# Kernel optimization log

Measured on AMD Instinct MI355X. Metric: run time of the kernel, lower is better.

## Reference

```python
import jax, jax.numpy as jnp
import numpy as np

DIM = 512
D_STATE = 16
D_CONV = 4
EXPAND = 2
D_INNER = EXPAND * DIM
DT_RANK = (DIM + 15) // 16  # ceil(dim/16) = 32
B_SZ, SEQ = 2, 2048


def _silu(v):
    return v * jax.nn.sigmoid(v)


def _mamba(x, in_w, conv_w, conv_b, xproj_w, dt_w, dt_b, A_log, D, out_w):
    """Single Mamba block forward (mamba_ssm reference math).
    x: [B, L, d_model]
    """
    Bb, L, _ = x.shape
    d_inner = conv_w.shape[0]
    d_state = A_log.shape[1]
    dt_rank = dt_w.shape[1]

    xz = x @ in_w.T                          # [B, L, 2*d_inner]
    xi, z = jnp.split(xz, 2, axis=-1)

    # causal depthwise conv1d (kernel D_CONV) + SiLU
    K = conv_w.shape[-1]
    xp = jnp.pad(xi, ((0, 0), (K - 1, 0), (0, 0)))
    xc = conv_b + sum(xp[:, k:k + L, :] * conv_w[:, 0, k] for k in range(K))
    xc = _silu(xc)                           # [B, L, d_inner]

    x_dbl = xc @ xproj_w.T                   # [B, L, dt_rank + 2*d_state]
    dt = x_dbl[..., :dt_rank]
    Bm = x_dbl[..., dt_rank:dt_rank + d_state]
    Cm = x_dbl[..., dt_rank + d_state:]
    dt = jax.nn.softplus(dt @ dt_w.T + dt_b)  # [B, L, d_inner]

    A = -jnp.exp(A_log)                      # [d_inner, d_state]
    dA = jnp.exp(dt[..., None] * A)          # [B, L, d_inner, d_state]
    dBu = (dt * xc)[..., None] * Bm[:, :, None, :]

    def step(h, inp):
        dA_t, dBu_t, C_t = inp
        h = dA_t * h + dBu_t                 # [B, d_inner, d_state]
        y = jnp.einsum('bds,bs->bd', h, C_t)
        return h, y

    h0 = jnp.zeros((Bb, d_inner, d_state), dtype=x.dtype)
    _, ys = jax.lax.scan(
        step, h0,
        (dA.transpose(1, 0, 2, 3), dBu.transpose(1, 0, 2, 3), Cm.transpose(1, 0, 2)))
    y = ys.transpose(1, 0, 2) + D * xc       # skip connection via D
    y = y * _silu(z)
    return y @ out_w.T                       # [B, L, d_model]


def _make_mamba_params(key):
    ks = jax.random.split(key, 7)
    s = 0.02
    in_w = jax.random.normal(ks[0], (2 * D_INNER, DIM), jnp.float32) * s
    conv_w = jax.random.normal(ks[1], (D_INNER, 1, D_CONV), jnp.float32) * 0.2
    conv_b = jnp.zeros((D_INNER,), jnp.float32)
    xproj_w = jax.random.normal(ks[2], (DT_RANK + 2 * D_STATE, D_INNER), jnp.float32) * s
    dt_w = jax.random.normal(ks[3], (D_INNER, DT_RANK), jnp.float32) * (DT_RANK ** -0.5)
    dt_b = jax.random.uniform(ks[4], (D_INNER,), jnp.float32, -4.0, -2.0)  # small softplus(dt)
    A_log = jnp.log(jnp.broadcast_to(jnp.arange(1, D_STATE + 1, dtype=jnp.float32), (D_INNER, D_STATE)))
    D = jnp.ones((D_INNER,), jnp.float32)
    out_w = jax.random.normal(ks[5], (DIM, D_INNER), jnp.float32) * s
    return (in_w, conv_w, conv_b, xproj_w, dt_w, dt_b, A_log, D, out_w)


def setup_inputs() -> dict:
    key = jax.random.key(0)
    kx, kf, kr = jax.random.split(key, 3)
    x = jax.random.normal(kx, (B_SZ, SEQ, DIM), jnp.float32)
    f = _make_mamba_params(kf)
    r = _make_mamba_params(kr)
    names = ['in_w', 'conv_w', 'conv_b', 'xproj_w', 'dt_w', 'dt_b', 'A_log', 'D', 'out_w']
    d = {'x': x}
    for n, v in zip(names, f):
        d['f_' + n] = v
    for n, v in zip(names, r):
        d['r_' + n] = v
    return d


def reference(x,
              f_in_w, f_conv_w, f_conv_b, f_xproj_w, f_dt_w, f_dt_b, f_A_log, f_D, f_out_w,
              r_in_w, r_conv_w, r_conv_b, r_xproj_w, r_dt_w, r_dt_b, r_A_log, r_D, r_out_w):
    x_f = _mamba(x, f_in_w, f_conv_w, f_conv_b, f_xproj_w, f_dt_w, f_dt_b, f_A_log, f_D, f_out_w)
    xr = jnp.flip(x, axis=1)
    x_r = jnp.flip(_mamba(xr, r_in_w, r_conv_w, r_conv_b, r_xproj_w, r_dt_w, r_dt_b, r_A_log, r_D, r_out_w), axis=1)
    return (x_f + x_r) * 0.5
```

## Files before the change

kernel.cpp:

```cpp
#include <hip/hip_runtime.h>
#include <hip/hip_bf16.h>
#include <math.h>

#define DIM      512
#define D_STATE  16
#define D_CONV   4
#define D_INNER  1024
#define DT_RANK  32
#define B_SZ     2
#define SEQ      2048
#define NTOK     (B_SZ * SEQ)
#define CHUNK    64
#define NCH      (SEQ / CHUNK)
#define NC_PAD   1152
#define PG       8
#define NPG      (CHUNK / PG)

#define XCB_STR   4194304
#define WCB_STR   1179648
#define BC_STR    131072
#define CH_STR    1048576

typedef __attribute__((ext_vector_type(8))) short bf16x8;
typedef __attribute__((ext_vector_type(4))) float f32x4;

__device__ __forceinline__ short f2bf(float f) {
    unsigned u = __float_as_uint(f);
    u += 0x7fffu + ((u >> 16) & 1u);
    return (short)(u >> 16);
}
__device__ __forceinline__ float bf2f(short v) {
    return __uint_as_float(((unsigned)(unsigned short)v) << 16);
}
__device__ __forceinline__ float softplus_fast(float v) {
    return (v > 20.f) ? v : __logf(1.f + __expf(v));
}

__global__ __launch_bounds__(256)
void cvt_bf16(const float* __restrict__ src, short* __restrict__ dst, int n)
{
    int i = (blockIdx.x * 256 + threadIdx.x) * 8;
    if (i >= n) return;
    float4 a = *(const float4*)(src + i);
    float4 b = *(const float4*)(src + i + 4);
    bf16x8 v;
    v[0] = f2bf(a.x); v[1] = f2bf(a.y); v[2] = f2bf(a.z); v[3] = f2bf(a.w);
    v[4] = f2bf(b.x); v[5] = f2bf(b.y); v[6] = f2bf(b.z); v[7] = f2bf(b.w);
    *(bf16x8*)(dst + i) = v;
}

__global__ __launch_bounds__(256)
void cvt_wcat(const float* __restrict__ wf, const float* __restrict__ wr,
              short* __restrict__ Wcat)
{
    int idx = blockIdx.x * 256 + threadIdx.x;
    if (idx >= 512 * 2048) return;
    int n = idx >> 11, col = idx & 2047;
    const float* src = (col < 1024) ? wf : wr;
    Wcat[idx] = f2bf(src[n * 1024 + (col & 1023)]);
}

__global__ __launch_bounds__(256)
void build_wc(const float* __restrict__ xp0, const float* __restrict__ xp1,
              const float* __restrict__ dw0, const float* __restrict__ dw1,
              short* __restrict__ Wcb)
{
    const int dir = blockIdx.y;
    int idx = blockIdx.x * 256 + threadIdx.x;
    if (idx >= NC_PAD * D_INNER) return;
    const float* xproj_w = dir ? xp1 : xp0;
    const float* dt_w    = dir ? dw1 : dw0;
    int i = idx >> 10, k = idx & 1023;
    float v;
    if (i < 1024) {
        v = 0.f;
#pragma unroll
        for (int r = 0; r < 32; ++r)
            v = fmaf(dt_w[i * 32 + r], xproj_w[r * 1024 + k], v);
    } else if (i < 1056) {
        v = xproj_w[(i - 1024 + 32) * 1024 + k];
    } else {
        v = 0.f;
    }
    Wcb[(size_t)dir * WCB_STR + idx] = f2bf(v);
}

template<int CFG>
__global__ __launch_bounds__(256)
void gemm_bf16(const short* __restrict__ A, const short* __restrict__ A2,
               int lda, int K1,
               const short* __restrict__ W, int ldw,
               void* __restrict__ Cv, int ldc,
               int K, float alpha, int cmode,
               const float* __restrict__ dtb0, const float* __restrict__ dtb1,
               float* __restrict__ BCb, int aStr, int wStr)
{
    constexpr int TMc = CFG ? 64 : 128;
    constexpr int TKc = CFG ? 64 : 32;
    constexpr int WTS = CFG ? 32 : 64;
    constexpr int FC  = CFG ? 2 : 4;
    __shared__ __align__(16) short As[2][TMc * TKc];
    __shared__ __align__(16) short Ws[2][TMc * TKc];

    const int nx = gridDim.x, ny = gridDim.y;
    const int nwg = nx * ny * gridDim.z;
    int lin = blockIdx.x + nx * (blockIdx.y + ny * blockIdx.z);
    int swz = (lin & 7) * (nwg >> 3) + (lin >> 3);
    const int bx = swz % nx;
    int tmp = swz / nx;
    const int by = tmp % ny;
    const int dir = tmp / ny;

    A  += (size_t)dir * aStr;
    A2 += (size_t)dir * aStr;
    W  += (size_t)dir * wStr;

    const int tid  = threadIdx.x;
    const int lane = tid & 63;
    const int wid  = tid >> 6;
    const int wr   = wid >> 1, wc = wid & 1;
    const int m0 = by * TMc;
    const int n0 = bx * TMc;

    const int am0 = CFG ? (((tid >> 7) << 4) | (tid & 15))
                        : (((tid >> 6) << 4) | (tid & 15));
    const int kc0 = CFG ? ((tid >> 4) & 7) : ((tid >> 4) & 3);
    const int rstep = CFG ? 32 : 64;
    const size_t arow0 = (size_t)(m0 + am0) * lda + kc0 * 8;
    const size_t arow1 = arow0 + (size_t)rstep * lda;
    const short* pw0 = W + (size_t)(n0 + am0) * ldw + kc0 * 8;
    const short* pw1 = pw0 + (size_t)rstep * ldw;

    const int ci0 = tid, ci1 = tid + 256;

    f32x4 acc[FC][FC] = {};
    const int nt = K / TKc;

    bf16x8 ra0, ra1, rw0, rw1;

#define LOADR(tt) do {                                          \
    const int off_ = (tt) * TKc;                                \
    const short* ab_ = (off_ < K1) ? A : A2;                    \
    const int ao_ = (off_ < K1) ? off_ : off_ - K1;             \
    ra0 = *(const bf16x8*)(ab_ + arow0 + ao_);                  \
    ra1 = *(const bf16x8*)(ab_ + arow1 + ao_);                  \
    rw0 = *(const bf16x8*)(pw0 + off_);                         \
    rw1 = *(const bf16x8*)(pw1 + off_); } while (0)

#define DSWRITE(buf) do {                                       \
    *(bf16x8*)(As[buf] + ci0 * 8) = ra0;                        \
    *(bf16x8*)(As[buf] + ci1 * 8) = ra1;                        \
    *(bf16x8*)(Ws[buf] + ci0 * 8) = rw0;                        \
    *(bf16x8*)(Ws[buf] + ci1 * 8) = rw1; } while (0)

    LOADR(0);
    DSWRITE(0);
    LOADR(1);
    __syncthreads();

    for (int t = 0; t < nt; ++t) {
        const int cur = t & 1;
        if (t + 1 < nt) DSWRITE(cur ^ 1);
        if (t + 2 < nt) LOADR(t + 2);

        if constexpr (CFG == 0) {
            bf16x8 af[4], bff[4];
#pragma unroll
            for (int f = 0; f < 4; ++f) {
                int ai = (wr * 4 + f) * 64 + (lane >> 4) * 16 + (lane & 15);
                af[f]  = *(const bf16x8*)(&As[cur][ai * 8]);
                int bi = (wc * 4 + f) * 64 + (lane >> 4) * 16 + (lane & 15);
                bff[f] = *(const bf16x8*)(&Ws[cur][bi * 8]);
            }
#pragma unroll
            for (int i = 0; i < 4; ++i)
#pragma unroll
                for (int j = 0; j < 4; ++j)
                    acc[i][j] = __builtin_amdgcn_mfma_f32_16x16x32_bf16(
                        af[i], bff[j], acc[i][j], 0, 0, 0);
        } else {
            bf16x8 af[2][2], bff[2][2];
#pragma unroll
            for (int f = 0; f < 2; ++f)
#pragma unroll
                for (int ks = 0; ks < 2; ++ks) {
                    int ai = (wr * 2 + f) * 128 + ks * 64 + (lane >> 4) * 16 + (lane & 15);
                    af[f][ks] = *(const bf16x8*)(&As[cur][ai * 8]);
                    int bi = (wc * 2 + f) * 128 + ks * 64 + (lane >> 4) * 16 + (lane & 15);
                    bff[f][ks] = *(const bf16x8*)(&Ws[cur][bi * 8]);
                }
#pragma unroll
            for (int i = 0; i < 2; ++i)
#pragma unroll
                for (int j = 0; j < 2; ++j) {
                    acc[i][j] = __builtin_amdgcn_mfma_f32_16x16x32_bf16(
                        af[i][0], bff[j][0], acc[i][j], 0, 0, 0);
                    acc[i][j] = __builtin_amdgcn_mfma_f32_16x16x32_bf16(
                        af[i][1], bff[j][1], acc[i][j], 0, 0, 0);
                }
        }
        __syncthreads();
    }
#undef LOADR
#undef DSWRITE

    if (cmode == 2) {
        short* C = (short*)Cv;
#pragma unroll
        for (int i = 0; i < FC; ++i) {
            int row = m0 + wr * WTS + i * 16 + ((lane >> 4) << 2);
#pragma unroll
            for (int j = 0; j < FC; ++j) {
                int col = n0 + wc * WTS + j * 16 + (lane & 15);
#pragma unroll
                for (int r = 0; r < 4; ++r)
                    C[(size_t)(row + r) * ldc + col] = f2bf(alpha * acc[i][j][r]);
            }
        }
    } else if (cmode == 3) {
        if (n0 < 1024) {
            short* dtO = (short*)Cv;
            const float* dtb = dir ? dtb1 : dtb0;
#pragma unroll
            for (int i = 0; i < FC; ++i) {
                int row = m0 + wr * WTS + i * 16 + ((lane >> 4) << 2);
#pragma unroll
                for (int j = 0; j < FC; ++j) {
                    int col = n0 + wc * WTS + j * 16 + (lane & 15);
                    float bias = dtb[col];
#pragma unroll
                    for (int r = 0; r < 4; ++r) {
                        float v = softplus_fast(acc[i][j][r] + bias);
                        dtO[(size_t)(row + r) * 4096 + dir * 2048 + col] = f2bf(v);
                    }
                }
            }
        } else {
            float* bc = BCb + (size_t)dir * BC_STR;
#pragma unroll
            for (int i = 0; i < FC; ++i) {
                int row = m0 + wr * WTS + i * 16 + ((lane >> 4) << 2);
#pragma unroll
                for (int j = 0; j < FC; ++j) {
                    int col = n0 + wc * WTS + j * 16 + (lane & 15);
                    if (col < 1056) {
#pragma unroll
                        for (int r = 0; r < 4; ++r)
                            bc[(size_t)(row + r) * 32 + (col - 1024)] = acc[i][j][r];
                    }
                }
            }
        }
    } else {
        float* C = (float*)Cv;
#pragma unroll
        for (int i = 0; i < FC; ++i) {
            int row = m0 + wr * WTS + i * 16 + ((lane >> 4) << 2);
#pragma unroll
            for (int j = 0; j < FC; ++j) {
                int col = n0 + wc * WTS + j * 16 + (lane & 15);
#pragma unroll
                for (int r = 0; r < 4; ++r)
                    C[(size_t)(row + r) * ldc + col] = alpha * acc[i][j][r];
            }
        }
    }
}

__global__ __launch_bounds__(256)
void conv_silu_kernel(const short* __restrict__ xzb,
                      const float* __restrict__ cw0, const float* __restrict__ cw1,
                      const float* __restrict__ cb0, const float* __restrict__ cb1,
                      short* __restrict__ xcb)
{
    const int rev = blockIdx.y;
    int idx = blockIdx.x * 256 + threadIdx.x;
    if (idx >= NTOK * D_INNER) return;
    int c   = idx & (D_INNER - 1);
    int row = idx >> 10;
    int b   = row / SEQ;
    int u   = row - b * SEQ;
    const int coff = rev * 2048 + c;
    const float* cw = rev ? cw1 : cw0;
    const float* cb = rev ? cb1 : cb0;

    float w0 = cw[c * 4 + 0], w1 = cw[c * 4 + 1];
    float w2 = cw[c * 4 + 2], w3 = cw[c * 4 + 3];
    float accv = cb[c];
    if (!rev) {
#pragma unroll
        for (int k = 0; k < 4; ++k) {
            int uu = u - 3 + k;
            float wv = (k == 0) ? w0 : (k == 1) ? w1 : (k == 2) ? w2 : w3;
            if (uu >= 0)
                accv = fmaf(wv, bf2f(xzb[(size_t)(b * SEQ + uu) * 4096 + coff]), accv);
        }
    } else {
#pragma unroll
        for (int k = 0; k < 4; ++k) {
            int uu = u + 3 - k;
            float wv = (k == 0) ? w0 : (k == 1) ? w1 : (k == 2) ? w2 : w3;
            if (uu < SEQ)
                accv = fmaf(wv, bf2f(xzb[(size_t)(b * SEQ + uu) * 4096 + coff]), accv);
        }
    }
    float r = accv / (1.f + __expf(-accv));
    xcb[(size_t)rev * XCB_STR + idx] = f2bf(r);
}

__global__ __launch_bounds__(256)
void scan_p1(const short* __restrict__ xzb,
             const short* __restrict__ xcb,
             const float* __restrict__ BCb,
             const float* __restrict__ A_log0, const float* __restrict__ A_log1,
             float* __restrict__ chP, float* __restrict__ chH)
{
    __shared__ float Bs[CHUNK][16];
    const int tid = threadIdx.x;
    const int blk = blockIdx.x;
    const int dir = blk >> 8;
    const int rr  = blk & 255;
    const int cb = rr & 3;
    const int ch = (rr >> 2) & (NCH - 1);
    const int b  = rr >> 7;
    const int c  = cb * 256 + tid;
    const int rev = dir;

    const int u0 = rev ? (SEQ - 1 - ch * CHUNK) : (ch * CHUNK);
    const int st = rev ? -1 : 1;
    const float* A_log = dir ? A_log1 : A_log0;
    const float* bcD = BCb + (size_t)dir * BC_STR;

    for (int r = tid; r < CHUNK * 16; r += 256) {
        int i = r >> 4, s = r & 15;
        int row = b * SEQ + u0 + st * i;
        Bs[i][s] = bcD[(size_t)row * 32 + s];
    }

    float Acs[16];
#pragma unroll
    for (int s = 0; s < 16; ++s)
        Acs[s] = -__expf(A_log[c * 16 + s]) * 1.44269504f;

    float h[16];
    float dts = 0.f;
#pragma unroll
    for (int s = 0; s < 16; ++s) h[s] = 0.f;

    __syncthreads();

    const short* dtp = xzb + (size_t)(b * SEQ + u0) * 4096 + dir * 2048 + c;
    const short* xcp = xcb + (size_t)dir * XCB_STR + (size_t)(b * SEQ + u0) * D_INNER + c;
    const ptrdiff_t dstep = (ptrdiff_t)st * 4096;
    const ptrdiff_t xstep = (ptrdiff_t)st * D_INNER;

    float dt_r[PG], xc_r[PG];
#pragma unroll
    for (int j = 0; j < PG; ++j) {
        dt_r[j] = bf2f(dtp[dstep * j]);
        xc_r[j] = bf2f(xcp[xstep * j]);
    }

#pragma unroll 1
    for (int g = 0; g < NPG; ++g) {
        const int gg = (g + 1 < NPG) ? (g + 1) : g;
        float dt_n[PG], xc_n[PG];
#pragma unroll
        for (int j = 0; j < PG; ++j) {
            int i = gg * PG + j;
            dt_n[j] = bf2f(dtp[dstep * i]);
            xc_n[j] = bf2f(xcp[xstep * i]);
        }
#pragma unroll
        for (int j = 0; j < PG; ++j) {
            int i = g * PG + j;
            float dtv = dt_r[j];
            float e = dtv * xc_r[j];
            dts += dtv;
#pragma unroll
            for (int s = 0; s < 16; ++s) {
                float da = __builtin_amdgcn_exp2f(dtv * Acs[s]);
                h[s] = fmaf(da, h[s], e * Bs[i][s]);
            }
        }
#pragma unroll
        for (int j = 0; j < PG; ++j) { dt_r[j] = dt_n[j]; xc_r[j] = xc_n[j]; }
    }

    size_t o = (size_t)dir * CH_STR + ((size_t)(b * NCH + ch) * 1024 + c) * 16;
#pragma unroll
    for (int q = 0; q < 4; ++q) {
        float4 pv;
        pv.x = __builtin_amdgcn_exp2f(Acs[q*4+0] * dts);
        pv.y = __builtin_amdgcn_exp2f(Acs[q*4+1] * dts);
        pv.z = __builtin_amdgcn_exp2f(Acs[q*4+2] * dts);
        pv.w = __builtin_amdgcn_exp2f(Acs[q*4+3] * dts);
        *(float4*)&chP[o + q * 4] = pv;
        *(float4*)&chH[o + q * 4] = make_float4(h[q*4], h[q*4+1], h[q*4+2], h[q*4+3]);
    }
}

__global__ __launch_bounds__(256)
void scan_p2(float* __restrict__ chPH, const float* __restrict__ chH)
{
    int idx = blockIdx.x * 256 + threadIdx.x;
    int dir = idx >> 15;
    int rem = idx & 32767;
    int b  = rem >> 14;
    int cs = rem & 16383;
    size_t base = (size_t)dir * CH_STR;
    float h = 0.f;
#pragma unroll
    for (int ch = 0; ch < NCH; ++ch) {
        size_t o = base + ((size_t)(b * NCH + ch) << 14) + cs;
        float Pv = chPH[o], Hv = chH[o];
        chPH[o] = h;
        h = fmaf(Pv, h, Hv);
    }
}

__global__ __launch_bounds__(256)
void scan_p3(const short* __restrict__ xzb,
             short* __restrict__ xcb,
             const float* __restrict__ BCb,
             const float* __restrict__ A_log0, const float* __restrict__ A_log1,
             const float* __restrict__ Dp0, const float* __restrict__ Dp1,
             const float* __restrict__ hst)
{
    __shared__ float Bs[CHUNK][16];
    __shared__ float Cs[CHUNK][16];
    const int tid = threadIdx.x;
    const int blk = blockIdx.x;
    const int dir = blk >> 8;
    const int rr  = blk & 255;
    const int cb = rr & 3;
    const int ch = (rr >> 2) & (NCH - 1);
    const int b  = rr >> 7;
    const int c  = cb * 256 + tid;
    const int rev = dir;

    const int u0 = rev ? (SEQ - 1 - ch * CHUNK) : (ch * CHUNK);
    const int st = rev ? -1 : 1;
    const float* A_log = dir ? A_log1 : A_log0;
    const float* Dp    = dir ? Dp1 : Dp0;
    const float* bcD = BCb + (size_t)dir * BC_STR;

    for (int r = tid; r < CHUNK * 16; r += 256) {
        int i = r >> 4, s = r & 15;
        int row = b * SEQ + u0 + st * i;
        Bs[i][s] = bcD[(size_t)row * 32 + s];
        Cs[i][s] = bcD[(size_t)row * 32 + 16 + s];
    }

    float Acs[16];
#pragma unroll
    for (int s = 0; s < 16; ++s)
        Acs[s] = -__expf(A_log[c * 16 + s]) * 1.44269504f;

    const float Dc = Dp[c];

    float h[16];
    size_t o = (size_t)dir * CH_STR + ((size_t)(b * NCH + ch) * 1024 + c) * 16;
#pragma unroll
    for (int q = 0; q < 4; ++q) {
        float4 hv = *(const float4*)&hst[o + q * 4];
        h[q*4] = hv.x; h[q*4+1] = hv.y; h[q*4+2] = hv.z; h[q*4+3] = hv.w;
    }

    __syncthreads();

    const short* dtp = xzb + (size_t)(b * SEQ + u0) * 4096 + dir * 2048 + c;
    const short* zp  = xzb + (size_t)(b * SEQ + u0) * 4096 + dir * 2048 + 1024 + c;
    short*       xcp = xcb + (size_t)dir * XCB_STR + (size_t)(b * SEQ + u0) * D_INNER + c;
    const ptrdiff_t dstep = (ptrdiff_t)st * 4096;
    const ptrdiff_t xstep = (ptrdiff_t)st * D_INNER;

    float dt_r[PG], xc_r[PG], z_r[PG];
#pragma unroll
    for (int j = 0; j < PG; ++j) {
        dt_r[j] = bf2f(dtp[dstep * j]);
        xc_r[j] = bf2f(xcp[xstep * j]);
        z_r[j]  = bf2f(zp[dstep * j]);
    }

#pragma unroll 1
    for (int g = 0; g < NPG; ++g) {
        const int gg = (g + 1 < NPG) ? (g + 1) : g;
        float dt_n[PG], xc_n[PG], z_n[PG];
#pragma unroll
        for (int j = 0; j < PG; ++j) {
            int i = gg * PG + j;
            dt_n[j] = bf2f(dtp[dstep * i]);
            xc_n[j] = bf2f(xcp[xstep * i]);
            z_n[j]  = bf2f(zp[dstep * i]);
        }
#pragma unroll
        for (int j = 0; j < PG; ++j) {
            int i = g * PG + j;
            float dtv = dt_r[j];
            float xcv = xc_r[j];
            float e = dtv * xcv;
            float y = 0.f;
#pragma unroll
            for (int s = 0; s < 16; ++s) {
                float da = __builtin_amdgcn_exp2f(dtv * Acs[s]);
                h[s] = fmaf(da, h[s], e * Bs[i][s]);
                y = fmaf(h[s], Cs[i][s], y);
            }
            y = fmaf(Dc, xcv, y);
            float zv = z_r[j];
            float sig = 1.f / (1.f + __expf(-zv));
            xcp[xstep * i] = f2bf(y * zv * sig);
        }
#pragma unroll
        for (int j = 0; j < PG; ++j) {
            dt_r[j] = dt_n[j]; xc_r[j] = xc_n[j]; z_r[j] = z_n[j];
        }
    }
}

extern "C" void kernel_launch(void* const* d_in, const int* in_sizes, int n_in,
                              void* d_out, int out_size, void* d_ws, size_t ws_size,
                              hipStream_t stream)
{
    const float* x = (const float*)d_in[0];
    float* out = (float*)d_out;
    float* ws  = (float*)d_ws;

    short* xzb  = (short*)ws;
    float* BCb  = ws + 8388608;
    float* chP  = ws + 8650752;
    float* chH  = ws + 10747904;
    short* Wcb  = (short*)(ws + 12845056);
    short* xbf  = (short*)(ws + 14024704);
    short* W1b  = (short*)(ws + 15073280);
    short* Wcat = (short*)(ws + 16121856);
    short* xcb  = (short*)(ws + 16646144);

    const int gElem = (NTOK * D_INNER + 255) / 256;

    cvt_bf16<<<(NTOK * DIM / 8 + 255) / 256, 256, 0, stream>>>(x, xbf, NTOK * DIM);
    cvt_bf16<<<(2 * D_INNER * DIM / 8 + 255) / 256, 256, 0, stream>>>(
        (const float*)d_in[1 + 0 * 9 + 0], W1b, 2 * D_INNER * DIM);
    cvt_bf16<<<(2 * D_INNER * DIM / 8 + 255) / 256, 256, 0, stream>>>(
        (const float*)d_in[1 + 1 * 9 + 0], W1b + 2 * D_INNER * DIM, 2 * D_INNER * DIM);
    cvt_wcat<<<(512 * 2048 + 255) / 256, 256, 0, stream>>>(
        (const float*)d_in[1 + 0 * 9 + 8], (const float*)d_in[1 + 1 * 9 + 8], Wcat);
    {
        dim3 g((NC_PAD * D_INNER + 255) / 256, 2);
        build_wc<<<g, 256, 0, stream>>>(
            (const float*)d_in[1 + 0 * 9 + 3], (const float*)d_in[1 + 1 * 9 + 3],
            (const float*)d_in[1 + 0 * 9 + 4], (const float*)d_in[1 + 1 * 9 + 4],
            Wcb);
    }

    {
        dim3 g(4096 / 128, NTOK / 128, 1);
        gemm_bf16<0><<<g, 256, 0, stream>>>(xbf, xbf, DIM, DIM, W1b, DIM,
                                            xzb, 4096, DIM, 1.f, 2,
                                            nullptr, nullptr, nullptr, 0, 0);
    }
    {
        dim3 g(gElem, 2);
        conv_silu_kernel<<<g, 256, 0, stream>>>(
            xzb,
            (const float*)d_in[1 + 0 * 9 + 1], (const float*)d_in[1 + 1 * 9 + 1],
            (const float*)d_in[1 + 0 * 9 + 2], (const float*)d_in[1 + 1 * 9 + 2],
            xcb);
    }
    {
        dim3 g(NC_PAD / 128, NTOK / 128, 2);
        gemm_bf16<0><<<g, 256, 0, stream>>>(xcb, xcb, D_INNER, D_INNER,
                                            Wcb, D_INNER,
                                            xzb, 0, D_INNER, 1.f, 3,
                                            (const float*)d_in[1 + 0 * 9 + 5],
                                            (const float*)d_in[1 + 1 * 9 + 5],
                                            BCb, XCB_STR, WCB_STR);
    }
    scan_p1<<<512, 256, 0, stream>>>(xzb, xcb, BCb,
                                     (const float*)d_in[1 + 0 * 9 + 6],
                                     (const float*)d_in[1 + 1 * 9 + 6],
                                     chP, chH);
    scan_p2<<<(2 * B_SZ * 16384) / 256, 256, 0, stream>>>(chP, chH);
    scan_p3<<<512, 256, 0, stream>>>(xzb, xcb, BCb,
                                     (const float*)d_in[1 + 0 * 9 + 6],
                                     (const float*)d_in[1 + 1 * 9 + 6],
                                     (const float*)d_in[1 + 0 * 9 + 7],
                                     (const float*)d_in[1 + 1 * 9 + 7],
                                     chP);
    {
        dim3 g(DIM / 64, NTOK / 64, 1);
        gemm_bf16<1><<<g, 256, 0, stream>>>(xcb, xcb + XCB_STR, D_INNER, D_INNER,
                                            Wcat, 2 * D_INNER,
                                            out, DIM, 2 * D_INNER, 0.5f, 0,
                                            nullptr, nullptr, nullptr, 0, 0);
    }
}
```

Before: 253.8 us.

## Load GEMM A fragments straight from global into registers, skipping LDS staging

In the large-tile GEMM configuration, the A operand is no longer staged through shared memory. Each wave loads its MFMA A fragments directly from global memory into registers, double-buffered across two K-steps. Only W is still staged in LDS. This removes the LDS writes and reads for A and halves the shared footprint, which could raise occupancy. In exchange, the global A loads are less coalesced, the K1/A2 split path is dropped for this configuration, and the loop assumes an even number of K tiles.

```diff
diff --git a/kernel.cpp b/kernel.cpp
--- a/kernel.cpp
+++ b/kernel.cpp
@@ -99,8 +99,6 @@
     constexpr int TKc = CFG ? 64 : 32;
     constexpr int WTS = CFG ? 32 : 64;
     constexpr int FC  = CFG ? 2 : 4;
-    __shared__ __align__(16) short As[2][TMc * TKc];
-    __shared__ __align__(16) short Ws[2][TMc * TKc];
 
     const int nx = gridDim.x, ny = gridDim.y;
     const int nwg = nx * ny * gridDim.z;
@@ -122,21 +120,87 @@
     const int m0 = by * TMc;
     const int n0 = bx * TMc;
 
-    const int am0 = CFG ? (((tid >> 7) << 4) | (tid & 15))
-                        : (((tid >> 6) << 4) | (tid & 15));
-    const int kc0 = CFG ? ((tid >> 4) & 7) : ((tid >> 4) & 3);
-    const int rstep = CFG ? 32 : 64;
-    const size_t arow0 = (size_t)(m0 + am0) * lda + kc0 * 8;
-    const size_t arow1 = arow0 + (size_t)rstep * lda;
-    const short* pw0 = W + (size_t)(n0 + am0) * ldw + kc0 * 8;
-    const short* pw1 = pw0 + (size_t)rstep * ldw;
-
-    const int ci0 = tid, ci1 = tid + 256;
-
     f32x4 acc[FC][FC] = {};
     const int nt = K / TKc;
 
-    bf16x8 ra0, ra1, rw0, rw1;
+    if constexpr (CFG == 0) {
+        __shared__ __align__(16) short Ws[2][TMc * TKc];
+
+        const int am0 = ((tid >> 6) << 4) | (tid & 15);
+        const int kc0 = (tid >> 4) & 3;
+        const short* pw0 = W + (size_t)(n0 + am0) * ldw + kc0 * 8;
+        const short* pw1 = pw0 + (size_t)64 * ldw;
+        const int ci0 = tid, ci1 = tid + 256;
+
+        const short* paf = A + (size_t)(m0 + wr * 64 + (lane & 15)) * lda
+                             + ((lane >> 4) << 3);
+        const size_t fstep = (size_t)16 * lda;
+
+        bf16x8 rw0, rw1, afA[4], afB[4];
+
+#define LOADW(tt) do { const int o_ = (tt) * TKc;                    \
+        rw0 = *(const bf16x8*)(pw0 + o_);                            \
+        rw1 = *(const bf16x8*)(pw1 + o_); } while (0)
+#define WSTAGE(buf) do {                                             \
+        *(bf16x8*)(Ws[buf] + ci0 * 8) = rw0;                         \
+        *(bf16x8*)(Ws[buf] + ci1 * 8) = rw1; } while (0)
+#define LOADAF(tt, dst) do { const int o_ = (tt) * TKc;              \
+        dst[0] = *(const bf16x8*)(paf + o_);                         \
+        dst[1] = *(const bf16x8*)(paf + fstep + o_);                 \
+        dst[2] = *(const bf16x8*)(paf + 2 * fstep + o_);             \
+        dst[3] = *(const bf16x8*)(paf + 3 * fstep + o_); } while (0)
+#define COMPUTE(afX, buf) do {                                       \
+        bf16x8 bff[4];                                               \
+        _Pragma("unroll")                                            \
+        for (int f = 0; f < 4; ++f) {                                \
+            int bi = (wc * 4 + f) * 64 + (lane >> 4) * 16 + (lane & 15); \
+            bff[f] = *(const bf16x8*)(&Ws[buf][bi * 8]);             \
+        }                                                            \
+        _Pragma("unroll")                                            \
+        for (int i = 0; i < 4; ++i)                                  \
+            _Pragma("unroll")                                        \
+            for (int j = 0; j < 4; ++j)                              \
+                acc[i][j] = __builtin_amdgcn_mfma_f32_16x16x32_bf16( \
+                    afX[i], bff[j], acc[i][j], 0, 0, 0); } while (0)
+
+        LOADW(0);
+        WSTAGE(0);
+        LOADW(1);
+        LOADAF(0, afA);
+        __syncthreads();
+
+        for (int t = 0; t < nt; t += 2) {
+            WSTAGE(1);
+            if (t + 2 < nt) LOADW(t + 2);
+            LOADAF(t + 1, afB);
+            COMPUTE(afA, 0);
+            __syncthreads();
+            if (t + 2 < nt) {
+                WSTAGE(0);
+                if (t + 3 < nt) LOADW(t + 3);
+                LOADAF(t + 2, afA);
+            }
+            COMPUTE(afB, 1);
+            __syncthreads();
+        }
+#undef LOADW
+#undef WSTAGE
+#undef LOADAF
+#undef COMPUTE
+    } else {
+        __shared__ __align__(16) short As[2][TMc * TKc];
+        __shared__ __align__(16) short Ws[2][TMc * TKc];
+
+        const int am0 = ((tid >> 7) << 4) | (tid & 15);
+        const int kc0 = (tid >> 4) & 7;
+        const int rstep = 32;
+        const size_t arow0 = (size_t)(m0 + am0) * lda + kc0 * 8;
+        const size_t arow1 = arow0 + (size_t)rstep * lda;
+        const short* pw0 = W + (size_t)(n0 + am0) * ldw + kc0 * 8;
+        const short* pw1 = pw0 + (size_t)rstep * ldw;
+        const int ci0 = tid, ci1 = tid + 256;
+
+        bf16x8 ra0, ra1, rw0, rw1;
 
 #define LOADR(tt) do {                                          \
     const int off_ = (tt) * TKc;                                \
@@ -153,32 +217,16 @@
     *(bf16x8*)(Ws[buf] + ci0 * 8) = rw0;                        \
     *(bf16x8*)(Ws[buf] + ci1 * 8) = rw1; } while (0)
 
-    LOADR(0);
-    DSWRITE(0);
-    LOADR(1);
-    __syncthreads();
-
-    for (int t = 0; t < nt; ++t) {
-        const int cur = t & 1;
-        if (t + 1 < nt) DSWRITE(cur ^ 1);
-        if (t + 2 < nt) LOADR(t + 2);
-
-        if constexpr (CFG == 0) {
-            bf16x8 af[4], bff[4];
-#pragma unroll
-            for (int f = 0; f < 4; ++f) {
-                int ai = (wr * 4 + f) * 64 + (lane >> 4) * 16 + (lane & 15);
-                af[f]  = *(const bf16x8*)(&As[cur][ai * 8]);
-                int bi = (wc * 4 + f) * 64 + (lane >> 4) * 16 + (lane & 15);
-                bff[f] = *(const bf16x8*)(&Ws[cur][bi * 8]);
-            }
-#pragma unroll
-            for (int i = 0; i < 4; ++i)
-#pragma unroll
-                for (int j = 0; j < 4; ++j)
-                    acc[i][j] = __builtin_amdgcn_mfma_f32_16x16x32_bf16(
-                        af[i], bff[j], acc[i][j], 0, 0, 0);
-        } else {
+        LOADR(0);
+        DSWRITE(0);
+        LOADR(1);
+        __syncthreads();
+
+        for (int t = 0; t < nt; ++t) {
+            const int cur = t & 1;
+            if (t + 1 < nt) DSWRITE(cur ^ 1);
+            if (t + 2 < nt) LOADR(t + 2);
+
             bf16x8 af[2][2], bff[2][2];
 #pragma unroll
             for (int f = 0; f < 2; ++f)
@@ -198,11 +246,11 @@
                     acc[i][j] = __builtin_amdgcn_mfma_f32_16x16x32_bf16(
                         af[i][1], bff[j][1], acc[i][j], 0, 0, 0);
                 }
-        }
-        __syncthreads();
-    }
+            __syncthreads();
+        }
 #undef LOADR
 #undef DSWRITE
+    }
 
     if (cmode == 2) {
         short* C = (short*)Cv;
```

Result: slower. 291.2 us (+14.7%).
